# Kernel optimization log

Hardware: AMD Instinct MI355X
Metric: run time of the kernel (lower is better)

The kernel has to match this reference:

```python
import jax, jax.numpy as jnp
import numpy as np

H, C, D, F = 8, 1024, 128, 512  # num_heads, num_chanels, out_dim, featurs_dim
B = 16


def setup_inputs() -> dict:
    key = jax.random.key(0)
    ks = jax.random.split(key, 9)
    s = 0.02
    return {
        "x": jax.random.normal(ks[0], (B, C, F), jnp.float32),
        "Wk": jax.random.normal(ks[1], (F, H * D), jnp.float32) * s,
        "bk": jax.random.normal(ks[2], (H * D,), jnp.float32) * s,
        "Wq": jax.random.normal(ks[3], (F, H * D), jnp.float32) * s,
        "bq": jax.random.normal(ks[4], (H * D,), jnp.float32) * s,
        "Wv": jax.random.normal(ks[5], (F, H * D), jnp.float32) * s,
        "bv": jax.random.normal(ks[6], (H * D,), jnp.float32) * s,
        "Ww0": jax.random.normal(ks[7], (H * D, D), jnp.float32) * s,
        "bw0": jax.random.normal(ks[8], (D,), jnp.float32) * s,
    }


def reference(x, Wk, bk, Wq, bq, Wv, bv, Ww0, bw0):
    # Linear projections on last dim: [B, C, H*D]
    # NOTE: the original reshapes [B, C, H*D] -> [B, H, C, D] WITHOUT a permute,
    # which mixes channel/head axes; we replicate that exactly.
    k = (x @ Wk + bk).reshape(-1, H, C, D)
    q = (x @ Wq + bq).reshape(-1, H, C, D)
    v = (x @ Wv + bv).reshape(-1, H, C, D)
    scores = jnp.einsum('bhcf,bhdf->bhcd', q, k) / jnp.sqrt(jnp.float32(D))
    att = jax.nn.softmax(scores, axis=-1) - jnp.eye(C, dtype=scores.dtype)
    vals = jnp.einsum('bhcd,bhdf->bhcf', att, v)          # [B, H, C, D]
    vals = vals.transpose(0, 2, 1, 3).reshape(vals.shape[0], C, H * D)
    return vals @ Ww0 + bw0                                # [B, C, D]
```

## Files before the change

kernel.cpp:

```cpp
#include <hip/hip_runtime.h>
#include <hip/hip_bf16.h>
#include <cstdint>
#include <cstddef>

using u16 = unsigned short;
typedef __attribute__((ext_vector_type(4))) float f32x4;
typedef __attribute__((ext_vector_type(16))) float f32x16;
typedef __attribute__((ext_vector_type(8))) unsigned short u16x8;
typedef __attribute__((ext_vector_type(4))) unsigned short u16x4;
typedef __attribute__((ext_vector_type(2))) unsigned short u16x2;
typedef __attribute__((ext_vector_type(4))) unsigned int u32x4;
typedef __bf16 bfrag __attribute__((ext_vector_type(8)));

constexpr int Hn = 8, Cn = 1024, Dn = 128, Fn = 512, Bn = 16;
constexpr int M1 = Bn * Cn;

constexpr size_t OFF_XB  = 0;
constexpr size_t SZ_XB   = (size_t)M1 * Fn * 2;
constexpr size_t OFF_WT  = OFF_XB + SZ_XB;
constexpr size_t SZ_WT   = 3ull * 1024 * 512 * 2;
constexpr size_t OFF_W0T = OFF_WT + SZ_WT;
constexpr size_t SZ_W0T  = 128ull * 1024 * 2;
constexpr size_t OFF_Q   = OFF_W0T + SZ_W0T;
constexpr size_t SZ_P    = (size_t)Bn * Hn * Cn * Dn * 2;
constexpr size_t OFF_K   = OFF_Q + SZ_P;
constexpr size_t OFF_V   = OFF_K + SZ_P;
constexpr size_t OFF_ATT = OFF_V + SZ_P;

__device__ __forceinline__ float bf2f(u16 u) {
  unsigned int x = ((unsigned int)u) << 16;
  return __builtin_bit_cast(float, x);
}
__device__ __forceinline__ u16 f2bf(float f) {
  unsigned int u = __builtin_bit_cast(unsigned int, f);
  u += 0x7fffu + ((u >> 16) & 1u);
  return (u16)(u >> 16);
}
__device__ __forceinline__ f32x4 mfma16(bfrag a, bfrag b, f32x4 c) {
  return __builtin_amdgcn_mfma_f32_16x16x32_bf16(a, b, c, 0, 0, 0);
}
__device__ __forceinline__ f32x16 mfma32(bfrag a, bfrag b, f32x16 c) {
  return __builtin_amdgcn_mfma_f32_32x32x16_bf16(a, b, c, 0, 0, 0);
}
__device__ __forceinline__ void gload16(const void* g, void* lds) {
  __builtin_amdgcn_global_load_lds(
      (const __attribute__((address_space(1))) unsigned int*)g,
      (__attribute__((address_space(3))) unsigned int*)lds, 16, 0, 0);
}
__device__ __forceinline__ unsigned cvtpk(float lo, float hi) {
  unsigned r;
  asm("v_cvt_pk_bf16_f32 %0, %1, %2" : "=v"(r) : "v"(lo), "v"(hi));
  return r;
}
__device__ __forceinline__ float fexp2(float x) {
  float r;
  asm("v_exp_f32 %0, %1" : "=v"(r) : "v"(x));
  return r;
}

__global__ void cvt_bf16(const float* __restrict__ in, u16* __restrict__ out, int n) {
  int idx = (blockIdx.x * blockDim.x + threadIdx.x) * 8;
  if (idx < n) {
    float4 v0 = *(const float4*)(in + idx);
    float4 v1 = *(const float4*)(in + idx + 4);
    u16x8 o;
    o[0] = f2bf(v0.x); o[1] = f2bf(v0.y); o[2] = f2bf(v0.z); o[3] = f2bf(v0.w);
    o[4] = f2bf(v1.x); o[5] = f2bf(v1.y); o[6] = f2bf(v1.z); o[7] = f2bf(v1.w);
    *(u16x8*)(out + idx) = o;
  }
}

__global__ void transpose_cvt(const float* __restrict__ in, u16* __restrict__ out,
                              int R, int Cc) {
  __shared__ float tile[32][33];
  int c0 = blockIdx.x * 32, r0 = blockIdx.y * 32;
  int tx = threadIdx.x, ty = threadIdx.y;
#pragma unroll
  for (int i = 0; i < 4; ++i)
    tile[ty + i * 8][tx] = in[(size_t)(r0 + ty + i * 8) * Cc + c0 + tx];
  __syncthreads();
#pragma unroll
  for (int i = 0; i < 4; ++i)
    out[(size_t)(c0 + ty + i * 8) * R + r0 + tx] = f2bf(tile[tx][ty + i * 8]);
}

__global__ void transpose_cvt3(const float* __restrict__ W0, const float* __restrict__ W1,
                               const float* __restrict__ W2, u16* __restrict__ out) {
  __shared__ float tile[32][33];
  const int z = blockIdx.z;
  const float* in = (z == 0) ? W0 : (z == 1) ? W1 : W2;
  u16* op = out + (size_t)z * 1024 * 512;
  int c0 = blockIdx.x * 32, r0 = blockIdx.y * 32;
  int tx = threadIdx.x, ty = threadIdx.y;
#pragma unroll
  for (int i = 0; i < 4; ++i)
    tile[ty + i * 8][tx] = in[(size_t)(r0 + ty + i * 8) * 1024 + c0 + tx];
  __syncthreads();
#pragma unroll
  for (int i = 0; i < 4; ++i)
    op[(size_t)(c0 + ty + i * 8) * 512 + r0 + tx] = f2bf(tile[tx][ty + i * 8]);
}

__global__ void vtrans(const u16* __restrict__ in, u16* __restrict__ out) {
  __shared__ u16 tile[64][65];
  int d0 = blockIdx.x * 64, c0 = blockIdx.y * 64, bh = blockIdx.z;
  const u16* ip = in + (size_t)bh * (Cn * Dn);
  u16* op = out + (size_t)bh * (Dn * Cn);
  int tx = threadIdx.x, ty = threadIdx.y;
#pragma unroll
  for (int i = 0; i < 8; ++i) {
    int r = ty + i * 8;
    u16x2 v = *(const u16x2*)&ip[(size_t)(c0 + r) * Dn + d0 + tx * 2];
    tile[r][tx * 2] = v.x;
    tile[r][tx * 2 + 1] = v.y;
  }
  __syncthreads();
#pragma unroll
  for (int i = 0; i < 8; ++i) {
    int rr = ty + i * 8;
    u16x2 v;
    v.x = tile[tx * 2][rr];
    v.y = tile[tx * 2 + 1][rr];
    *(u16x2*)&op[(size_t)(d0 + rr) * Cn + c0 + tx * 2] = v;
  }
}

__global__ void qkv_gemm(const u16* __restrict__ xb, const u16* __restrict__ wt,
                         const float* __restrict__ bq, const float* __restrict__ bk,
                         const float* __restrict__ bv,
                         u16* __restrict__ qout, u16* __restrict__ kout,
                         u16* __restrict__ vout) {
  __shared__ u16 As[128 * 64];
  __shared__ u16 Bs[128 * 64];
  const int m0 = blockIdx.x * 128;
  const int n0 = blockIdx.y * 128;
  const int p  = blockIdx.z;
  const u16* wp = wt + (size_t)p * 1024 * 512;
  const float* bias = (p == 0) ? bq : (p == 1) ? bk : bv;
  u16* outp = (p == 0) ? qout : (p == 1) ? kout : vout;
  const float osc = (p == 0) ? 0.12751744116389548f : 1.0f;

  const int tid = threadIdx.x, l = tid & 63, w = tid >> 6;
  const int lr = l & 15, lg = l >> 4;
  const int wr = w >> 1, wc = w & 1;

  f32x4 acc[4][4] = {};

  for (int kt = 0; kt < Fn; kt += 64) {
#pragma unroll
    for (int i = 0; i < 4; ++i) {
      int chb = (i * 4 + w) * 64;
      int ch = chb + l;
      int row = ch >> 3, scc = (ch & 7) ^ (row & 7);
      gload16(xb + (size_t)(m0 + row) * Fn + kt + scc * 8, &As[chb * 8]);
    }
#pragma unroll
    for (int i = 0; i < 4; ++i) {
      int chb = (i * 4 + w) * 64;
      int ch = chb + l;
      int row = ch >> 3, scc = (ch & 7) ^ (row & 7);
      gload16(wp + (size_t)(n0 + row) * Fn + kt + scc * 8, &Bs[chb * 8]);
    }
    __syncthreads();
#pragma unroll
    for (int kk = 0; kk < 2; ++kk) {
      bfrag af[4], bf_[4];
#pragma unroll
      for (int fm = 0; fm < 4; ++fm) {
        int row = wr * 64 + fm * 16 + lr;
        int off = (kk * 4 + lg) ^ (row & 7);
        af[fm] = *(const bfrag*)&As[row * 64 + off * 8];
      }
#pragma unroll
      for (int fn = 0; fn < 4; ++fn) {
        int row = wc * 64 + fn * 16 + lr;
        int off = (kk * 4 + lg) ^ (row & 7);
        bf_[fn] = *(const bfrag*)&Bs[row * 64 + off * 8];
      }
#pragma unroll
      for (int fm = 0; fm < 4; ++fm)
#pragma unroll
        for (int fn = 0; fn < 4; ++fn)
          acc[fm][fn] = mfma16(af[fm], bf_[fn], acc[fm][fn]);
    }
    __syncthreads();
  }

#pragma unroll
  for (int fm = 0; fm < 4; ++fm) {
#pragma unroll
    for (int r = 0; r < 4; ++r) {
      int m = m0 + wr * 64 + fm * 16 + lg * 4 + r;
      int b = m >> 10, c = m & 1023;
      int gh = c >> 7;
#pragma unroll
      for (int fn = 0; fn < 4; ++fn) {
        int j = n0 + wc * 64 + fn * 16 + lr;
        float v = (acc[fm][fn][r] + bias[j]) * osc;
        int ii = ((c & 127) << 3) | (j >> 7);
        int d = j & 127;
        size_t idx = (((size_t)(b * 8 + gh) * 1024 + ii) << 7) | d;
        outp[idx] = f2bf(v);
      }
    }
  }
}

__global__ __launch_bounds__(512, 2)
void attn_kernel(const u16* __restrict__ qp_all, const u16* __restrict__ kp_all,
                 const u16* __restrict__ vt_all, u16* __restrict__ attout) {
  __shared__ u16 smem[2 * 16384];
  char* smb = (char*)smem;

  const int bid = blockIdx.x;
  const int wg = (bid & 7) * 64 + (bid >> 3);
  const int bh = wg >> 2;
  const int qtp = wg & 3;

  const int tid = threadIdx.x, l = tid & 63, w = tid >> 6;
  const int q31 = l & 31, hi = l >> 5;

  const u16* qp  = qp_all + (size_t)bh * (Cn * Dn);
  const u16* kp  = kp_all + (size_t)bh * (Cn * Dn);
  const u16* vtp = vt_all + (size_t)bh * (Dn * Cn);
  const int qr0 = qtp * 256 + w * 32;

  const unsigned LK = (unsigned)(q31 * 256) ^ (unsigned)((q31 & 15) * 16) ^ (unsigned)(hi * 16);
  const unsigned LV = 16384u ^ (unsigned)(q31 * 128) ^ (unsigned)((q31 & 7) * 16) ^ (unsigned)(hi * 16);

  const u16* ksrc[2]; const u16* vsrc[2];
  unsigned kdst[2], vdst[2];
#pragma unroll
  for (int c = 0; c < 2; ++c) {
    int ch = c * 512 + tid;
    int krow = ch >> 4, kscc = (ch & 15) ^ (krow & 15);
    ksrc[c] = kp + krow * 128 + kscc * 8;
    int vrow = ch >> 3, vscc = (ch & 7) ^ (vrow & 7);
    vsrc[c] = vtp + (size_t)vrow * 1024 + vscc * 8;
    kdst[c] = (unsigned)((c * 512 + w * 64) * 16);
    vdst[c] = 16384u + (unsigned)((c * 512 + w * 64) * 16);
  }
  auto stage = [&](int t2, unsigned bufb) {
#pragma unroll
    for (int c = 0; c < 2; ++c)
      gload16(ksrc[c] + (size_t)t2 * 8192, smb + (bufb ^ kdst[c]));
#pragma unroll
    for (int c = 0; c < 2; ++c)
      gload16(vsrc[c] + (size_t)t2 * 64, smb + (bufb ^ vdst[c]));
  };

  bfrag aq[8];
#pragma unroll
  for (int kk = 0; kk < 8; ++kk)
    aq[kk] = *(const bfrag*)(qp + (size_t)(qr0 + q31) * Dn + kk * 16 + hi * 8);

  f32x16 ot[4] = {};
  float lsum = 0.f;

  stage(0, 0);
  __syncthreads();

  unsigned bufb = 0;
  for (int t = 0; t < 16; ++t) {
    const unsigned nb = bufb ^ 32768u;
    if (t < 15) stage(t + 1, nb);
    const unsigned LKb = LK ^ bufb;
    const unsigned LVb = LV ^ bufb;

    f32x16 st0 = {}, st1 = {};
    __builtin_amdgcn_s_setprio(1);
#pragma unroll
    for (int kk = 0; kk < 8; ++kk) {
      bfrag k0 = *(const bfrag*)(smb + (LKb ^ (unsigned)(kk * 32)));
      st0 = mfma32(k0, aq[kk], st0);
      bfrag k1 = *(const bfrag*)(smb + (LKb ^ (unsigned)(8192 + kk * 32)));
      st1 = mfma32(k1, aq[kk], st1);
    }
    __builtin_amdgcn_s_setprio(0);

    float rp[4] = {0.f, 0.f, 0.f, 0.f};
#pragma unroll
    for (int r = 0; r < 16; ++r) {
      float p0 = fexp2(st0[r]);
      st0[r] = p0;
      rp[r & 3] += p0;
    }
#pragma unroll
    for (int r = 0; r < 16; ++r) {
      float p1 = fexp2(st1[r]);
      st1[r] = p1;
      rp[r & 3] += p1;
    }
    lsum += (rp[0] + rp[1]) + (rp[2] + rp[3]);

    bfrag pb[4];
    {
      unsigned c0_[8], c1_[8];
#pragma unroll
      for (int m = 0; m < 8; ++m) {
        c0_[m] = cvtpk(st0[2 * m], st0[2 * m + 1]);
        c1_[m] = cvtpk(st1[2 * m], st1[2 * m + 1]);
      }
#pragma unroll
      for (int kkt = 0; kkt < 2; ++kkt) {
        unsigned a0 = c0_[4 * kkt + 0], b0 = c0_[4 * kkt + 2];
        unsigned a1 = c0_[4 * kkt + 1], b1 = c0_[4 * kkt + 3];
        asm("v_permlane32_swap_b32 %0, %1" : "+v"(a0), "+v"(b0));
        asm("v_permlane32_swap_b32 %0, %1" : "+v"(a1), "+v"(b1));
        u32x4 bw; bw.x = a0; bw.y = a1; bw.z = b0; bw.w = b1;
        pb[kkt] = __builtin_bit_cast(bfrag, bw);
      }
#pragma unroll
      for (int kkt = 0; kkt < 2; ++kkt) {
        unsigned a0 = c1_[4 * kkt + 0], b0 = c1_[4 * kkt + 2];
        unsigned a1 = c1_[4 * kkt + 1], b1 = c1_[4 * kkt + 3];
        asm("v_permlane32_swap_b32 %0, %1" : "+v"(a0), "+v"(b0));
        asm("v_permlane32_swap_b32 %0, %1" : "+v"(a1), "+v"(b1));
        u32x4 bw; bw.x = a0; bw.y = a1; bw.z = b0; bw.w = b1;
        pb[2 + kkt] = __builtin_bit_cast(bfrag, bw);
      }
    }

    __builtin_amdgcn_s_setprio(1);
#pragma unroll
    for (int kk = 0; kk < 4; ++kk) {
#pragma unroll
      for (int dt = 0; dt < 4; ++dt) {
        bfrag vf = *(const bfrag*)(smb + (LVb ^ (unsigned)(dt * 4096 + kk * 32)));
        ot[dt] = mfma32(vf, pb[kk], ot[dt]);
      }
    }
    __builtin_amdgcn_s_setprio(0);
    __syncthreads();
    bufb = nb;
  }

  const float lfull = lsum + __shfl_xor(lsum, 32, 64);
  const float linv = 1.f / lfull;
  const int c1 = qr0 + q31;
  u16* my = smem + w * 4096;
#pragma unroll
  for (int dt = 0; dt < 4; ++dt)
#pragma unroll
    for (int rp2 = 0; rp2 < 8; ++rp2) {
      int reg = 2 * rp2;
      int d = dt * 32 + (reg & 3) + 8 * (reg >> 2) + 4 * hi;
      float v0 = bf2f(vtp[((size_t)d << 10) | c1]);
      float v1 = bf2f(vtp[((size_t)(d + 1) << 10) | c1]);
      unsigned pk = cvtpk(ot[dt][reg] * linv - v0, ot[dt][reg + 1] * linv - v1);
      *(unsigned*)&my[q31 * 128 + (((d >> 3) ^ (q31 & 7)) << 3) + (d & 7)] = pk;
    }
  const int b = bh >> 3, h = bh & 7;
#pragma unroll
  for (int it = 0; it < 8; ++it) {
    int rowq = it * 4 + (l >> 4);
    int ch = l & 15;
    u16x8 rd = *(const u16x8*)&my[rowq * 128 + ((ch ^ (rowq & 7))) * 8];
    int cg = qr0 + rowq;
    *(u16x8*)&attout[(((size_t)(b * 1024 + cg)) * 8 + h) * 128 + ch * 8] = rd;
  }
}

__global__ void out_gemm(const u16* __restrict__ A, const u16* __restrict__ Bt,
                         const float* __restrict__ bias, float* __restrict__ out) {
  __shared__ u16 As[32 * 64];
  __shared__ u16 Bs[128 * 64];
  const int m0 = blockIdx.x * 32;
  const int tid = threadIdx.x, l = tid & 63, w = tid >> 6;
  const int lr = l & 15, lg = l >> 4;
  f32x4 acc[2][2] = {};

  for (int kt = 0; kt < 1024; kt += 64) {
    {
      int ch = w * 64 + l;
      int row = ch >> 3, scc = (ch & 7) ^ (row & 7);
      gload16(A + (size_t)(m0 + row) * 1024 + kt + scc * 8, &As[(w * 64) * 8]);
    }
#pragma unroll
    for (int i = 0; i < 4; ++i) {
      int chb = (i * 4 + w) * 64;
      int ch = chb + l;
      int row = ch >> 3, scc = (ch & 7) ^ (row & 7);
      gload16(Bt + (size_t)row * 1024 + kt + scc * 8, &Bs[chb * 8]);
    }
    __syncthreads();
#pragma unroll
    for (int kk = 0; kk < 2; ++kk) {
      bfrag af[2], bf_[2];
#pragma unroll
      for (int fm = 0; fm < 2; ++fm) {
        int row = fm * 16 + lr;
        int off = (kk * 4 + lg) ^ (row & 7);
        af[fm] = *(const bfrag*)&As[row * 64 + off * 8];
      }
#pragma unroll
      for (int fn = 0; fn < 2; ++fn) {
        int row = w * 32 + fn * 16 + lr;
        int off = (kk * 4 + lg) ^ (row & 7);
        bf_[fn] = *(const bfrag*)&Bs[row * 64 + off * 8];
      }
#pragma unroll
      for (int fm = 0; fm < 2; ++fm)
#pragma unroll
        for (int fn = 0; fn < 2; ++fn)
          acc[fm][fn] = mfma16(af[fm], bf_[fn], acc[fm][fn]);
    }
    __syncthreads();
  }
#pragma unroll
  for (int fm = 0; fm < 2; ++fm)
#pragma unroll
    for (int r = 0; r < 4; ++r) {
      int m = m0 + fm * 16 + lg * 4 + r;
#pragma unroll
      for (int fn = 0; fn < 2; ++fn) {
        int j = w * 32 + fn * 16 + lr;
        out[(size_t)m * 128 + j] = acc[fm][fn][r] + bias[j];
      }
    }
}

extern "C" void kernel_launch(void* const* d_in, const int* in_sizes, int n_in,
                              void* d_out, int out_size, void* d_ws, size_t ws_size,
                              hipStream_t stream) {
  const float* x   = (const float*)d_in[0];
  const float* Wk  = (const float*)d_in[1];
  const float* bk_ = (const float*)d_in[2];
  const float* Wq  = (const float*)d_in[3];
  const float* bq_ = (const float*)d_in[4];
  const float* Wv  = (const float*)d_in[5];
  const float* bv_ = (const float*)d_in[6];
  const float* Ww0 = (const float*)d_in[7];
  const float* bw0 = (const float*)d_in[8];
  float* out = (float*)d_out;

  char* ws = (char*)d_ws;
  u16* xb   = (u16*)(ws + OFF_XB);
  u16* wt   = (u16*)(ws + OFF_WT);
  u16* w0t  = (u16*)(ws + OFF_W0T);
  u16* qpm  = (u16*)(ws + OFF_Q);
  u16* kpm  = (u16*)(ws + OFF_K);
  u16* vpm  = (u16*)(ws + OFF_V);
  u16* attb = (u16*)(ws + OFF_ATT);

  cvt_bf16<<<(M1 * Fn / 8 + 255) / 256, 256, 0, stream>>>(x, xb, M1 * Fn);
  dim3 tb(32, 8);
  transpose_cvt3<<<dim3(32, 16, 3), tb, 0, stream>>>(Wq, Wk, Wv, wt);
  transpose_cvt<<<dim3(4, 32), tb, 0, stream>>>(Ww0, w0t, 1024, 128);

  qkv_gemm<<<dim3(128, 8, 3), 256, 0, stream>>>(xb, wt, bq_, bk_, bv_, qpm, kpm, attb);

  vtrans<<<dim3(2, 16, 128), tb, 0, stream>>>(attb, vpm);

  attn_kernel<<<dim3(512), 512, 0, stream>>>(qpm, kpm, vpm, attb);

  out_gemm<<<512, 256, 0, stream>>>(attb, w0t, bw0, out);
}
```

Baseline: 179.1 us.

## Fuse V transpose into QKV GEMM epilogue and drop vtrans kernel

The V projection epilogue now transposes its 128x128 tile through shared memory and writes V directly in a transposed block layout. This removes the separate vtrans kernel launch and its full read/write pass over V. The attention kernel's K and V staging addresses and the residual V read are remapped to match the new layouts. The trade-off is extra shared-memory staging and a synchronisation in the GEMM epilogue for the V slice, plus more complex index mapping.

```diff
diff --git a/kernel.cpp b/kernel.cpp
--- a/kernel.cpp
+++ b/kernel.cpp
@@ -101,43 +101,19 @@
     op[(size_t)(c0 + ty + i * 8) * 512 + r0 + tx] = f2bf(tile[tx][ty + i * 8]);
 }
 
-__global__ void vtrans(const u16* __restrict__ in, u16* __restrict__ out) {
-  __shared__ u16 tile[64][65];
-  int d0 = blockIdx.x * 64, c0 = blockIdx.y * 64, bh = blockIdx.z;
-  const u16* ip = in + (size_t)bh * (Cn * Dn);
-  u16* op = out + (size_t)bh * (Dn * Cn);
-  int tx = threadIdx.x, ty = threadIdx.y;
-#pragma unroll
-  for (int i = 0; i < 8; ++i) {
-    int r = ty + i * 8;
-    u16x2 v = *(const u16x2*)&ip[(size_t)(c0 + r) * Dn + d0 + tx * 2];
-    tile[r][tx * 2] = v.x;
-    tile[r][tx * 2 + 1] = v.y;
-  }
-  __syncthreads();
-#pragma unroll
-  for (int i = 0; i < 8; ++i) {
-    int rr = ty + i * 8;
-    u16x2 v;
-    v.x = tile[tx * 2][rr];
-    v.y = tile[tx * 2 + 1][rr];
-    *(u16x2*)&op[(size_t)(d0 + rr) * Cn + c0 + tx * 2] = v;
-  }
-}
-
 __global__ void qkv_gemm(const u16* __restrict__ xb, const u16* __restrict__ wt,
                          const float* __restrict__ bq, const float* __restrict__ bk,
                          const float* __restrict__ bv,
                          u16* __restrict__ qout, u16* __restrict__ kout,
                          u16* __restrict__ vout) {
-  __shared__ u16 As[128 * 64];
-  __shared__ u16 Bs[128 * 64];
+  __shared__ u16 sAB[16384];
+  u16* As = sAB;
+  u16* Bs = sAB + 8192;
   const int m0 = blockIdx.x * 128;
   const int n0 = blockIdx.y * 128;
   const int p  = blockIdx.z;
   const u16* wp = wt + (size_t)p * 1024 * 512;
   const float* bias = (p == 0) ? bq : (p == 1) ? bk : bv;
-  u16* outp = (p == 0) ? qout : (p == 1) ? kout : vout;
   const float osc = (p == 0) ? 0.12751744116389548f : 1.0f;
 
   const int tid = threadIdx.x, l = tid & 63, w = tid >> 6;
@@ -186,6 +162,36 @@
     __syncthreads();
   }
 
+  if (p == 2) {
+    const int y = n0 >> 7;
+#pragma unroll
+    for (int fm = 0; fm < 4; ++fm) {
+#pragma unroll
+      for (int fn = 0; fn < 4; ++fn) {
+        int kb = wr * 64 + fm * 16 + lg * 4;
+        int d  = wc * 64 + fn * 16 + lr;
+        float b0 = bias[n0 + d];
+        unsigned p01 = cvtpk(acc[fm][fn][0] + b0, acc[fm][fn][1] + b0);
+        unsigned p23 = cvtpk(acc[fm][fn][2] + b0, acc[fm][fn][3] + b0);
+        int kx = kb ^ ((d & 7) << 3);
+        *(unsigned*)&sAB[d * 128 + kx]     = p01;
+        *(unsigned*)&sAB[d * 128 + kx + 2] = p23;
+      }
+    }
+    __syncthreads();
+    const int b = m0 >> 10, gh = (m0 & 1023) >> 7;
+    u16* outv = vout + ((size_t)((b * 8 + gh) * 8 + y)) * 16384;
+#pragma unroll
+    for (int i = 0; i < 8; ++i) {
+      int g = i * 256 + tid;
+      int d = g >> 4, s = g & 15;
+      u16x8 vv = *(const u16x8*)&sAB[d * 128 + ((s ^ (d & 7)) << 3)];
+      *(u16x8*)&outv[d * 128 + s * 8] = vv;
+    }
+    return;
+  }
+
+  u16* outp = (p == 0) ? qout : kout;
 #pragma unroll
   for (int fm = 0; fm < 4; ++fm) {
 #pragma unroll
@@ -234,9 +240,11 @@
   for (int c = 0; c < 2; ++c) {
     int ch = c * 512 + tid;
     int krow = ch >> 4, kscc = (ch & 15) ^ (krow & 15);
-    ksrc[c] = kp + krow * 128 + kscc * 8;
-    int vrow = ch >> 3, vscc = (ch & 7) ^ (vrow & 7);
-    vsrc[c] = vtp + (size_t)vrow * 1024 + vscc * 8;
+    int csrc = 8 * (krow & 7) + (krow >> 3);
+    ksrc[c] = kp + csrc * 128 + kscc * 8;
+    int vrow = ch >> 3;
+    int vy = (ch & 7) ^ (vrow & 7);
+    vsrc[c] = vtp + (size_t)vy * 16384 + vrow * 128;
     kdst[c] = (unsigned)((c * 512 + w * 64) * 16);
     vdst[c] = 16384u + (unsigned)((c * 512 + w * 64) * 16);
   }
@@ -246,7 +254,7 @@
       gload16(ksrc[c] + (size_t)t2 * 8192, smb + (bufb ^ kdst[c]));
 #pragma unroll
     for (int c = 0; c < 2; ++c)
-      gload16(vsrc[c] + (size_t)t2 * 64, smb + (bufb ^ vdst[c]));
+      gload16(vsrc[c] + (size_t)t2 * 8, smb + (bufb ^ vdst[c]));
   };
 
   bfrag aq[8];
@@ -338,6 +346,7 @@
   const float lfull = lsum + __shfl_xor(lsum, 32, 64);
   const float linv = 1.f / lfull;
   const int c1 = qr0 + q31;
+  const u16* vcol = vtp + (size_t)(c1 & 7) * 16384 + (c1 >> 3);
   u16* my = smem + w * 4096;
 #pragma unroll
   for (int dt = 0; dt < 4; ++dt)
@@ -345,8 +354,8 @@
     for (int rp2 = 0; rp2 < 8; ++rp2) {
       int reg = 2 * rp2;
       int d = dt * 32 + (reg & 3) + 8 * (reg >> 2) + 4 * hi;
-      float v0 = bf2f(vtp[((size_t)d << 10) | c1]);
-      float v1 = bf2f(vtp[((size_t)(d + 1) << 10) | c1]);
+      float v0 = bf2f(vcol[(size_t)d * 128]);
+      float v1 = bf2f(vcol[(size_t)(d + 1) * 128]);
       unsigned pk = cvtpk(ot[dt][reg] * linv - v0, ot[dt][reg + 1] * linv - v1);
       *(unsigned*)&my[q31 * 128 + (((d >> 3) ^ (q31 & 7)) << 3) + (d & 7)] = pk;
     }
@@ -448,9 +457,7 @@
   transpose_cvt3<<<dim3(32, 16, 3), tb, 0, stream>>>(Wq, Wk, Wv, wt);
   transpose_cvt<<<dim3(4, 32), tb, 0, stream>>>(Ww0, w0t, 1024, 128);
 
-  qkv_gemm<<<dim3(128, 8, 3), 256, 0, stream>>>(xb, wt, bq_, bk_, bv_, qpm, kpm, attb);
-
-  vtrans<<<dim3(2, 16, 128), tb, 0, stream>>>(attb, vpm);
+  qkv_gemm<<<dim3(128, 8, 3), 256, 0, stream>>>(xb, wt, bq_, bk_, bv_, qpm, kpm, vpm);
 
   attn_kernel<<<dim3(512), 512, 0, stream>>>(qpm, kpm, vpm, attb);
 
```

Result: no change. 176.5 us (-1.4%).
